# Optimization experiments

Measured on AMD Instinct MI355X. Metric: run time of the kernel, lower is better.

Reference implementation:

```python
import jax, jax.numpy as jnp
import numpy as np

T, B, IN_DIM = 8192, 4, 512
D_V, D_K, CHUNK = 512, 64, 128
EPS = 1e-8


def setup_inputs() -> dict:
    key = jax.random.key(0)
    ks = jax.random.split(key, 9)
    s = 0.02
    return {
        "x": jax.random.normal(ks[0], (T, B, IN_DIM), jnp.float32),
        "Wv": jax.random.normal(ks[1], (D_V, IN_DIM), jnp.float32) * s,
        "bv": jnp.zeros((D_V,), jnp.float32),
        "Wk": jax.random.normal(ks[2], (D_K, IN_DIM), jnp.float32) * s,
        "bk": jnp.zeros((D_K,), jnp.float32),
        "Wq": jax.random.normal(ks[3], (D_K, IN_DIM), jnp.float32) * s,
        "bq": jnp.zeros((D_K,), jnp.float32),
        "Wa": jax.random.normal(ks[4], (D_K, IN_DIM), jnp.float32) * s,
        "ba": jnp.zeros((D_K,), jnp.float32),
    }


def reference(x, Wv, bv, Wk, bk, Wq, bq, Wa, ba):
    # Projections: x (T, B, in_dim)
    v = x @ Wv.T + bv                      # (T, B, d)
    k = x @ Wk.T + bk                      # (T, B, n)
    q = x @ Wq.T + bq                      # (T, B, n)
    alpha = jax.nn.sigmoid(x @ Wa.T + ba)  # (T, B, n) decay gates

    Tt, Bb = x.shape[0], x.shape[1]
    C = CHUNK
    nC = Tt // C  # T assumed divisible by chunk size

    def to_chunks(a):
        return a.reshape(nC, C, Bb, a.shape[-1])

    vs, ks_, qs, als = to_chunks(v), to_chunks(k), to_chunks(q), to_chunks(alpha)
    causal = jnp.tril(jnp.ones((C, C), dtype=bool))  # (C, C)

    def body(S, inp):
        v_ch, k_ch, q_ch, a_ch = inp  # each (C, B, .)
        # Cumulative decay product within chunk (clamped as in the original)
        p = jnp.cumprod(jnp.maximum(a_ch, EPS), axis=0)      # (C, B, n)
        q_t = q_ch * p                                        # (C, B, n)
        k_t = k_ch / (p + EPS)                                # (C, B, n)
        # Intra-chunk causal attention scores
        A = jnp.einsum('tbn,sbn->bts', q_t, k_t)              # (B, C, C)
        A = jnp.where(causal[None, :, :], A, jnp.zeros((), A.dtype))
        y = jnp.einsum('bts,sbd->tbd', A, v_ch)               # intra-chunk
        y = y + jnp.einsum('bdn,tbn->tbd', S, q_t)            # cross-chunk carry
        # State update to end of chunk
        p_end = p[-1]                                         # (B, n)
        S_writes = jnp.einsum('tbd,tbn->bdn', v_ch, k_t * p_end[None, :, :])
        S_new = S * p_end[:, None, :] + S_writes              # (B, d, n)
        return S_new, y

    S0 = jnp.zeros((Bb, D_V, D_K), x.dtype)
    _, ys = jax.lax.scan(body, S0, (vs, ks_, qs, als))        # ys: (nC, C, B, d)
    return ys.reshape(Tt, Bb, D_V)
```

## Files before the change

### kernel.cpp

```cpp
#include <hip/hip_runtime.h>
#include <math.h>

#define T_DIM 8192
#define B_DIM 4
#define INDIM 512
#define DV 512
#define DK 64
#define CHUNK 128
#define NCH (T_DIM / CHUNK)
#define ROWS (T_DIM * B_DIM)
#define NPAD 768
#define KCAT 192
#define EPSF 1e-8f

typedef float float4_t __attribute__((ext_vector_type(4)));
typedef short short8_t __attribute__((ext_vector_type(8)));
typedef _Float16 half8_t __attribute__((ext_vector_type(8)));

__device__ inline unsigned short f2bf(float f) {
  unsigned int u = __float_as_uint(f);
  unsigned int r = (u + 0x7fffu + ((u >> 16) & 1u)) >> 16;
  return (unsigned short)r;
}
__device__ inline float bf2f(unsigned short h) {
  return __uint_as_float(((unsigned int)h) << 16);
}
__device__ inline unsigned short f2h(float f) {
  _Float16 h = (_Float16)f;
  unsigned short u;
  __builtin_memcpy(&u, &h, 2);
  return u;
}

__device__ inline void gload16(const void* g, void* l) {
  __builtin_amdgcn_global_load_lds(
      (const __attribute__((address_space(1))) void*)g,
      (__attribute__((address_space(3))) void*)l, 16, 0, 0);
}

__global__ __launch_bounds__(256) void cast_kernel(
    const float* __restrict__ x,
    const float* __restrict__ Wv, const float* __restrict__ Wk,
    const float* __restrict__ Wq, const float* __restrict__ Wa,
    const float* __restrict__ bv, const float* __restrict__ bk,
    const float* __restrict__ bq, const float* __restrict__ ba,
    unsigned short* __restrict__ xh, unsigned short* __restrict__ wh,
    float* __restrict__ bcat)
{
  if (blockIdx.x < 16384) {
    const size_t i4 = ((size_t)blockIdx.x * 256 + threadIdx.x) * 4;
    const float4 v = *(const float4*)&x[i4];
    ushort4 h;
    h.x = f2h(v.x); h.y = f2h(v.y); h.z = f2h(v.z); h.w = f2h(v.w);
    *(ushort4*)&xh[i4] = h;
  } else {
    const int t = (blockIdx.x - 16384) * 256 + threadIdx.x;
    const size_t i4 = (size_t)t * 4;
    const int row = (int)(i4 >> 9);
    const int col = (int)(i4 & 511);
    float4 v = {0.f, 0.f, 0.f, 0.f};
    if (row < 512)      v = *(const float4*)&Wv[(size_t)row * INDIM + col];
    else if (row < 576) v = *(const float4*)&Wk[(size_t)(row - 512) * INDIM + col];
    else if (row < 640) v = *(const float4*)&Wq[(size_t)(row - 576) * INDIM + col];
    else if (row < 704) v = *(const float4*)&Wa[(size_t)(row - 640) * INDIM + col];
    ushort4 h;
    h.x = f2h(v.x); h.y = f2h(v.y); h.z = f2h(v.z); h.w = f2h(v.w);
    *(ushort4*)&wh[i4] = h;
    if (t < NPAD) {
      float b = 0.f;
      if (t < 512)      b = bv[t];
      else if (t < 576) b = bk[t - 512];
      else if (t < 640) b = bq[t - 576];
      else if (t < 704) b = ba[t - 640];
      bcat[t] = b;
    }
  }
}

__global__ __launch_bounds__(256) void proj_mfma_kernel(
    const unsigned short* __restrict__ xh, const unsigned short* __restrict__ wh,
    const float* __restrict__ bcat,
    unsigned short* __restrict__ Bt_h, unsigned short* __restrict__ Bt_l,
    float* __restrict__ k_ws, float* __restrict__ q_ws,
    float* __restrict__ a_ws)
{
  __shared__ __align__(16) _Float16 Ah[3][128 * 32];
  __shared__ __align__(16) _Float16 Bh[3][128 * 32];

  const int d     = blockIdx.x;
  const int grp   = d >> 3;
  const int ytile = (d & 7) * 32 + grp / 6;
  const int xtile = grp % 6;
  const int r0 = ytile * 128;
  const int c0 = xtile * 128;

  const int tid  = threadIdx.x;
  const int wave = tid >> 6, lane = tid & 63;
  const int wm   = (wave & 1) * 64, wn = (wave >> 1) * 64;
  const int fm   = lane & 15;
  const int fk   = (lane >> 4) * 8;
  const int g    = lane >> 4;

  float4_t acc[4][4];
#pragma unroll
  for (int i = 0; i < 4; ++i)
#pragma unroll
    for (int j = 0; j < 4; ++j) acc[i][j] = (float4_t)0.0f;

  const int srow = tid >> 2;
  const int scol = (((tid & 3) ^ (srow & 3)) * 8);

  const unsigned short* pA0 = xh + (size_t)(r0 + srow) * INDIM + scol;
  const unsigned short* pA1 = xh + (size_t)(r0 + 64 + srow) * INDIM + scol;
  const unsigned short* pB0 = wh + (size_t)(c0 + srow) * INDIM + scol;
  const unsigned short* pB1 = wh + (size_t)(c0 + 64 + srow) * INDIM + scol;

  auto stage = [&](int buf, int k0) {
    gload16(pA0 + k0, &Ah[buf][tid * 8]);
    gload16(pA1 + k0, &Ah[buf][(256 + tid) * 8]);
    gload16(pB0 + k0, &Bh[buf][tid * 8]);
    gload16(pB1 + k0, &Bh[buf][(256 + tid) * 8]);
  };

  auto compute = [&](int buf) {
    half8_t a[4], b[4];
#pragma unroll
    for (int i = 0; i < 4; ++i) {
      const int r = wm + i * 16 + fm;
      a[i] = *(const half8_t*)&Ah[buf][r * 32 + ((g ^ (r & 3)) << 3)];
    }
#pragma unroll
    for (int j = 0; j < 4; ++j) {
      const int r = wn + j * 16 + fm;
      b[j] = *(const half8_t*)&Bh[buf][r * 32 + ((g ^ (r & 3)) << 3)];
    }
    __builtin_amdgcn_s_setprio(1);
#pragma unroll
    for (int i = 0; i < 4; ++i)
#pragma unroll
      for (int j = 0; j < 4; ++j)
        acc[i][j] = __builtin_amdgcn_mfma_f32_16x16x32_f16(a[i], b[j], acc[i][j], 0, 0, 0);
    __builtin_amdgcn_s_setprio(0);
  };

  stage(0, 0);
  stage(1, 32);
  int cur = 0;
  for (int t = 0; t < 14; ++t) {
    stage((cur + 2) % 3, (t + 2) * 32);
    asm volatile("s_waitcnt vmcnt(8)" ::: "memory");
    __builtin_amdgcn_s_barrier();
    compute(cur);
    __builtin_amdgcn_s_barrier();
    cur = (cur + 1) % 3;
  }
  asm volatile("s_waitcnt vmcnt(4)" ::: "memory");
  __builtin_amdgcn_s_barrier();
  compute(cur);
  cur = (cur + 1) % 3;
  asm volatile("s_waitcnt vmcnt(0)" ::: "memory");
  __builtin_amdgcn_s_barrier();
  compute(cur);

  if (xtile < 4) {
    unsigned int* Thl = (unsigned int*)&Ah[0][0];
    const int t0 = r0 >> 2;
    const int cb0 = (t0 >> 7) * 4;
    const int s0 = t0 & 127;
    __syncthreads();
    for (int bb = 0; bb < 4; ++bb) {
#pragma unroll
      for (int j = 0; j < 4; ++j) {
        const int d_loc = wn + j * 16 + fm;
        const float bias = bcat[c0 + d_loc];
#pragma unroll
        for (int i = 0; i < 4; ++i) {
          const int trow = (wm >> 2) + i * 4 + g;
          const float val = acc[i][j][bb] + bias;
          const unsigned short h = f2bf(val);
          const unsigned short l = f2bf(val - bf2f(h));
          Thl[d_loc * 34 + trow] = (unsigned int)h | ((unsigned int)l << 16);
        }
      }
      __syncthreads();
#pragma unroll
      for (int q2 = 0; q2 < 4; ++q2) {
        const int task = q2 * 256 + tid;
        const int dd = task >> 3;
        const int tq = task & 7;
        const unsigned int* p = &Thl[dd * 34 + tq * 4];
        const unsigned int w0 = p[0], w1 = p[1], w2 = p[2], w3 = p[3];
        ushort4 hh, ll;
        hh.x = (unsigned short)w0; ll.x = (unsigned short)(w0 >> 16);
        hh.y = (unsigned short)w1; ll.y = (unsigned short)(w1 >> 16);
        hh.z = (unsigned short)w2; ll.z = (unsigned short)(w2 >> 16);
        hh.w = (unsigned short)w3; ll.w = (unsigned short)(w3 >> 16);
        const size_t oa = ((size_t)(cb0 + bb) * DV + c0 + dd) * CHUNK + s0 + tq * 4;
        *(ushort4*)&Bt_h[oa] = hh;
        *(ushort4*)&Bt_l[oa] = ll;
      }
      __syncthreads();
    }
  } else {
#pragma unroll
    for (int j = 0; j < 4; ++j) {
      const int col = c0 + wn + j * 16 + fm;
      if (col >= 704) continue;
      const float bias = bcat[col];
#pragma unroll
      for (int i = 0; i < 4; ++i) {
#pragma unroll
        for (int r = 0; r < 4; ++r) {
          const int row = r0 + wm + i * 16 + g * 4 + r;
          const float val = acc[i][j][r] + bias;
          if (col < 576) {
            k_ws[(size_t)row * DK + col - 512] = val;
          } else if (col < 640) {
            q_ws[(size_t)row * DK + col - 576] = val;
          } else {
            a_ws[(size_t)row * DK + col - 640] = 1.0f / (1.0f + expf(-val));
          }
        }
      }
    }
  }
}

__global__ __launch_bounds__(512) void prep_kernel(
    const float* __restrict__ a_ws, const float* __restrict__ k_ws,
    const float* __restrict__ q_ws,
    unsigned short* __restrict__ Acat_h, unsigned short* __restrict__ Acat_l,
    unsigned short* __restrict__ kT_h, unsigned short* __restrict__ kT_l,
    float* __restrict__ pend)
{
  __shared__ float pal[CHUNK][DK];
  __shared__ __align__(16) unsigned short Aq_h[128 * 64];
  __shared__ __align__(16) unsigned short Aq_l[128 * 64];
  __shared__ __align__(16) unsigned short Bk_h[128 * 64];
  __shared__ __align__(16) unsigned short Bk_l[128 * 64];

  const int bd = blockIdx.x;
  const int l  = (bd & 7) * 32 + (bd >> 3);
  const int c = l >> 2, b = l & 3;
  const int cb = c * B_DIM + b;
  const int tid = threadIdx.x;
  const int wave = tid >> 6, lane = tid & 63;
  const int wm = (wave & 1) * 64, wn = (wave >> 1) * 32;
  const int fm = lane & 15;
  const int fk = (lane >> 4) * 8;
  const int g  = lane >> 4;

#pragma unroll
  for (int i = 0; i < 4; ++i) {
    const int f = (i * 512 + tid) * 4;
    const int t = f >> 6, n0 = f & 63;
    const float4 av = *(const float4*)&a_ws[(size_t)(c * CHUNK + t) * 256 + b * 64 + n0];
    *(float4*)&pal[t][n0] = av;
  }
  __syncthreads();

  if (tid < 64) {
    float p = 1.0f;
#pragma unroll 4
    for (int t = 0; t < CHUNK; ++t) {
      p *= fmaxf(pal[t][tid], EPSF);
      pal[t][tid] = p;
    }
    pend[c * 256 + b * 64 + tid] = p;
  }
  __syncthreads();

#pragma unroll
  for (int i = 0; i < 4; ++i) {
    const int f = (i * 512 + tid) * 4;
    const int t = f >> 6, n0 = f & 63;
    const float4 qv = *(const float4*)&q_ws[(size_t)(c * CHUNK + t) * 256 + b * 64 + n0];
    const size_t qa = ((size_t)cb * CHUNK + t) * KCAT + 128 + n0;
    float q0 = qv.x * pal[t][n0 + 0];
    float q1 = qv.y * pal[t][n0 + 1];
    float q2 = qv.z * pal[t][n0 + 2];
    float q3 = qv.w * pal[t][n0 + 3];
    ushort4 h, l4;
    h.x = f2bf(q0); l4.x = f2bf(q0 - bf2f(h.x));
    h.y = f2bf(q1); l4.y = f2bf(q1 - bf2f(h.y));
    h.z = f2bf(q2); l4.z = f2bf(q2 - bf2f(h.z));
    h.w = f2bf(q3); l4.w = f2bf(q3 - bf2f(h.w));
    *(ushort4*)&Acat_h[qa] = h;
    *(ushort4*)&Acat_l[qa] = l4;
    const int wi = t * 64 + (n0 ^ ((t & 7) << 3));
    *(ushort4*)&Aq_h[wi] = h;
    *(ushort4*)&Aq_l[wi] = l4;
  }

#pragma unroll
  for (int i = 0; i < 4; ++i) {
    const int f = (i * 512 + tid) * 4;
    const int t = f >> 6, n0 = f & 63;
    const float4 kv = *(const float4*)&k_ws[(size_t)(c * CHUNK + t) * 256 + b * 64 + n0];
    float k0 = kv.x / (pal[t][n0 + 0] + EPSF);
    float k1 = kv.y / (pal[t][n0 + 1] + EPSF);
    float k2 = kv.z / (pal[t][n0 + 2] + EPSF);
    float k3 = kv.w / (pal[t][n0 + 3] + EPSF);
    ushort4 h, l4;
    h.x = f2bf(k0); l4.x = f2bf(k0 - bf2f(h.x));
    h.y = f2bf(k1); l4.y = f2bf(k1 - bf2f(h.y));
    h.z = f2bf(k2); l4.z = f2bf(k2 - bf2f(h.z));
    h.w = f2bf(k3); l4.w = f2bf(k3 - bf2f(h.w));
    const int wi = t * 64 + (n0 ^ ((t & 7) << 3));
    *(ushort4*)&Bk_h[wi] = h;
    *(ushort4*)&Bk_l[wi] = l4;
  }
  __syncthreads();

#pragma unroll
  for (int it = 0; it < 2; ++it) {
    const int task = it * 512 + tid;
    const int n  = task >> 4;
    const int tg = task & 15;
    ushort4 h0, h1, l0, l1;
    unsigned short hh[8], ll[8];
#pragma unroll
    for (int e = 0; e < 8; ++e) {
      const int wi = (tg * 8 + e) * 64 + (n ^ (e << 3));
      hh[e] = Bk_h[wi];
      ll[e] = Bk_l[wi];
    }
    h0.x = hh[0]; h0.y = hh[1]; h0.z = hh[2]; h0.w = hh[3];
    h1.x = hh[4]; h1.y = hh[5]; h1.z = hh[6]; h1.w = hh[7];
    l0.x = ll[0]; l0.y = ll[1]; l0.z = ll[2]; l0.w = ll[3];
    l1.x = ll[4]; l1.y = ll[5]; l1.z = ll[6]; l1.w = ll[7];
    const size_t oa = ((size_t)cb * DK + n) * CHUNK + tg * 8;
    *(ushort4*)&kT_h[oa]     = h0;
    *(ushort4*)&kT_h[oa + 4] = h1;
    *(ushort4*)&kT_l[oa]     = l0;
    *(ushort4*)&kT_l[oa + 4] = l1;
  }

  float4_t acc[4][2];
#pragma unroll
  for (int i = 0; i < 4; ++i)
#pragma unroll
    for (int j = 0; j < 2; ++j) acc[i][j] = (float4_t)0.0f;

#pragma unroll
  for (int ksub = 0; ksub < 2; ++ksub) {
    short8_t a_hi[4], a_lo[4], b_hi[2], b_lo[2];
#pragma unroll
    for (int i = 0; i < 4; ++i) {
      const int r = wm + i * 16 + fm;
      const int ar = r * 64 + ((ksub * 32 + fk) ^ ((r & 7) << 3));
      a_hi[i] = *(const short8_t*)&Aq_h[ar];
      a_lo[i] = *(const short8_t*)&Aq_l[ar];
    }
#pragma unroll
    for (int j = 0; j < 2; ++j) {
      const int r = wn + j * 16 + fm;
      const int br = r * 64 + ((ksub * 32 + fk) ^ ((r & 7) << 3));
      b_hi[j] = *(const short8_t*)&Bk_h[br];
      b_lo[j] = *(const short8_t*)&Bk_l[br];
    }
    __builtin_amdgcn_s_setprio(1);
#pragma unroll
    for (int i = 0; i < 4; ++i)
#pragma unroll
      for (int j = 0; j < 2; ++j) {
        acc[i][j] = __builtin_amdgcn_mfma_f32_16x16x32_bf16(a_hi[i], b_hi[j], acc[i][j], 0, 0, 0);
        acc[i][j] = __builtin_amdgcn_mfma_f32_16x16x32_bf16(a_lo[i], b_hi[j], acc[i][j], 0, 0, 0);
        acc[i][j] = __builtin_amdgcn_mfma_f32_16x16x32_bf16(a_hi[i], b_lo[j], acc[i][j], 0, 0, 0);
      }
    __builtin_amdgcn_s_setprio(0);
  }

#pragma unroll
  for (int j = 0; j < 2; ++j) {
    const int s = wn + j * 16 + fm;
#pragma unroll
    for (int i = 0; i < 4; ++i) {
#pragma unroll
      for (int r = 0; r < 4; ++r) {
        const int t = wm + i * 16 + g * 4 + r;
        const float vv = (s <= t) ? acc[i][j][r] : 0.0f;
        const unsigned short h = f2bf(vv);
        const size_t oa = ((size_t)cb * CHUNK + t) * KCAT + s;
        Acat_h[oa] = h;
        Acat_l[oa] = f2bf(vv - bf2f(h));
      }
    }
  }
}

__global__ __launch_bounds__(256) void wchunk_mfma_kernel(
    const unsigned short* __restrict__ Bt_h, const unsigned short* __restrict__ Bt_l,
    const unsigned short* __restrict__ kT_h, const unsigned short* __restrict__ kT_l,
    const float* __restrict__ pend, float* __restrict__ W_ws)
{
  __shared__ __align__(16) unsigned short Ah[128 * 32];
  __shared__ __align__(16) unsigned short Al[128 * 32];
  __shared__ __align__(16) unsigned short Kh[64 * 128];
  __shared__ __align__(16) unsigned short Kl[64 * 128];

  const int bd = blockIdx.x;
  const int u  = (bd & 7) * 128 + (bd >> 3);
  const int cb = u >> 2;
  const int dt = u & 3;
  const int tid  = threadIdx.x;
  const int wave = tid >> 6, lane = tid & 63;
  const int wm   = (wave & 1) * 64;
  const int wn   = (wave >> 1) * 32;
  const int fm   = lane & 15;
  const int fk   = (lane >> 4) * 8;
  const int g    = lane >> 4;

  const unsigned short* Ab_h = Bt_h + ((size_t)cb * DV + dt * 128) * CHUNK;
  const unsigned short* Ab_l = Bt_l + ((size_t)cb * DV + dt * 128) * CHUNK;
  const unsigned short* Kb_h = kT_h + (size_t)cb * DK * CHUNK;
  const unsigned short* Kb_l = kT_l + (size_t)cb * DK * CHUNK;

#pragma unroll
  for (int it = 0; it < 4; ++it) {
    const int tk = it * 256 + tid;
    const int n = tk >> 4, slot = tk & 15;
    gload16(&Kb_h[(size_t)n * CHUNK + ((slot ^ (n & 15)) << 3)], &Kh[tk * 8]);
    gload16(&Kb_l[(size_t)n * CHUNK + ((slot ^ (n & 15)) << 3)], &Kl[tk * 8]);
  }

  float4_t acc[4][2];
#pragma unroll
  for (int i = 0; i < 4; ++i)
#pragma unroll
    for (int j = 0; j < 2; ++j) acc[i][j] = (float4_t)0.0f;

  for (int ks = 0; ks < 4; ++ks) {
    const int k0 = ks * 32;
#pragma unroll
    for (int q = 0; q < 2; ++q) {
      const int flat = (q * 256 + tid) * 8;
      const int row = flat >> 5;
      const int col = (((tid & 3) ^ ((tid >> 2) & 3)) << 3);
      gload16(&Ab_h[(size_t)row * CHUNK + k0 + col], &Ah[flat]);
      gload16(&Ab_l[(size_t)row * CHUNK + k0 + col], &Al[flat]);
    }
    __syncthreads();

    short8_t a_hi[4], a_lo[4], b_hi[2], b_lo[2];
#pragma unroll
    for (int i = 0; i < 4; ++i) {
      const int r = wm + i * 16 + fm;
      const int ar = r * 32 + ((g ^ (r & 3)) << 3);
      a_hi[i] = *(const short8_t*)&Ah[ar];
      a_lo[i] = *(const short8_t*)&Al[ar];
    }
#pragma unroll
    for (int j = 0; j < 2; ++j) {
      const int n = wn + j * 16 + fm;
      const int slot = (k0 + fk) >> 3;
      const int addr = n * CHUNK + ((slot ^ (n & 15)) << 3);
      b_hi[j] = *(const short8_t*)&Kh[addr];
      b_lo[j] = *(const short8_t*)&Kl[addr];
    }
#pragma unroll
    for (int i = 0; i < 4; ++i)
#pragma unroll
      for (int j = 0; j < 2; ++j) {
        acc[i][j] = __builtin_amdgcn_mfma_f32_16x16x32_bf16(a_hi[i], b_hi[j], acc[i][j], 0, 0, 0);
        acc[i][j] = __builtin_amdgcn_mfma_f32_16x16x32_bf16(a_lo[i], b_hi[j], acc[i][j], 0, 0, 0);
        acc[i][j] = __builtin_amdgcn_mfma_f32_16x16x32_bf16(a_hi[i], b_lo[j], acc[i][j], 0, 0, 0);
      }
    __syncthreads();
  }

#pragma unroll
  for (int j = 0; j < 2; ++j) {
    const int n = wn + j * 16 + fm;
    const float pj = pend[(cb >> 2) * 256 + (cb & 3) * 64 + n];
#pragma unroll
    for (int i = 0; i < 4; ++i) {
#pragma unroll
      for (int r = 0; r < 4; ++r) {
        const int dd = dt * 128 + wm + i * 16 + (lane >> 4) * 4 + r;
        W_ws[((size_t)cb * DV + dd) * DK + n] = acc[i][j][r] * pj;
      }
    }
  }
}

__global__ __launch_bounds__(256) void scan_kernel(
    const float* __restrict__ W_ws, const float* __restrict__ pend,
    unsigned short* __restrict__ Sh, unsigned short* __restrict__ Sl)
{
  const int flat = blockIdx.x * 256 + threadIdx.x;
  const int n = flat & 63;
  const int b = flat >> 15;
  float s = 0.0f;
  float w0 = W_ws[flat];
  float w1 = W_ws[131072 + flat];
  for (int c = 0; c < NCH; c += 2) {
    const float wa = w0, wb = w1;
    if (c + 2 < NCH) w0 = W_ws[(size_t)(c + 2) * 131072 + flat];
    if (c + 3 < NCH) w1 = W_ws[(size_t)(c + 3) * 131072 + flat];
    unsigned short h = f2bf(s);
    Sh[(size_t)c * 131072 + flat] = h;
    Sl[(size_t)c * 131072 + flat] = f2bf(s - bf2f(h));
    s = s * pend[c * 256 + b * 64 + n] + wa;
    h = f2bf(s);
    Sh[(size_t)(c + 1) * 131072 + flat] = h;
    Sl[(size_t)(c + 1) * 131072 + flat] = f2bf(s - bf2f(h));
    s = s * pend[(c + 1) * 256 + b * 64 + n] + wb;
  }
}

__global__ __launch_bounds__(256) void out_mfma_kernel(
    const unsigned short* __restrict__ Acat_h, const unsigned short* __restrict__ Acat_l,
    const unsigned short* __restrict__ Bt_h, const unsigned short* __restrict__ Bt_l,
    const unsigned short* __restrict__ Sh, const unsigned short* __restrict__ Sl,
    float* __restrict__ out)
{
  __shared__ __align__(16) unsigned short Ah[128 * 64];
  __shared__ __align__(16) unsigned short Al[128 * 64];
  __shared__ __align__(16) unsigned short Bh[128 * 64];
  __shared__ __align__(16) unsigned short Bl[128 * 64];

  const int bd = blockIdx.x;
  const int cb = (bd >> 5) * 8 + (bd & 7);
  const int nt = (bd >> 3) & 3;
  const int c = cb >> 2, b = cb & 3;
  const int tid  = threadIdx.x;
  const int wave = tid >> 6, lane = tid & 63;
  const int wm   = (wave & 1) * 64, wn = (wave >> 1) * 64;
  const int fm   = lane & 15;
  const int fk   = (lane >> 4) * 8;

  const unsigned short* Ab_h = Acat_h + (size_t)cb * CHUNK * KCAT;
  const unsigned short* Ab_l = Acat_l + (size_t)cb * CHUNK * KCAT;
  const unsigned short* Bb_h = Bt_h + ((size_t)cb * DV + nt * 128) * CHUNK;
  const unsigned short* Bb_l = Bt_l + ((size_t)cb * DV + nt * 128) * CHUNK;
  const unsigned short* Sb_h = Sh + ((size_t)cb * DV + nt * 128) * DK;
  const unsigned short* Sb_l = Sl + ((size_t)cb * DV + nt * 128) * DK;

  const int srow = tid >> 3;
  const int scolB = (tid & 7) * 16;
  const int sc = (scolB ^ ((srow & 7) << 4)) >> 1;
  const int sdst = srow * 64 + (scolB >> 1);

  float4_t acc[4][4];
#pragma unroll
  for (int i = 0; i < 4; ++i)
#pragma unroll
    for (int j = 0; j < 4; ++j) acc[i][j] = (float4_t)0.0f;

  for (int ks = 0; ks < 3; ++ks) {
    const int k0 = ks * 64;
#pragma unroll
    for (int q = 0; q < 4; ++q) {
      const int row = q * 32 + srow;
      const int dst = q * 2048 + sdst;
      gload16(&Ab_h[(size_t)row * KCAT + k0 + sc], &Ah[dst]);
      gload16(&Ab_l[(size_t)row * KCAT + k0 + sc], &Al[dst]);
      if (ks < 2) {
        gload16(&Bb_h[(size_t)row * CHUNK + k0 + sc], &Bh[dst]);
        gload16(&Bb_l[(size_t)row * CHUNK + k0 + sc], &Bl[dst]);
      } else {
        gload16(&Sb_h[(size_t)row * DK + sc], &Bh[dst]);
        gload16(&Sb_l[(size_t)row * DK + sc], &Bl[dst]);
      }
    }
    __syncthreads();

#pragma unroll
    for (int ksub = 0; ksub < 2; ++ksub) {
      short8_t a_hi[4], a_lo[4], b_hi[4], b_lo[4];
#pragma unroll
      for (int i = 0; i < 4; ++i) {
        const int r = wm + i * 16 + fm;
        const int ar = r * 64 + ((ksub * 32 + fk) ^ ((r & 7) << 3));
        a_hi[i] = *(const short8_t*)&Ah[ar];
        a_lo[i] = *(const short8_t*)&Al[ar];
      }
#pragma unroll
      for (int j = 0; j < 4; ++j) {
        const int r = wn + j * 16 + fm;
        const int br = r * 64 + ((ksub * 32 + fk) ^ ((r & 7) << 3));
        b_hi[j] = *(const short8_t*)&Bh[br];
        b_lo[j] = *(const short8_t*)&Bl[br];
      }
      __builtin_amdgcn_s_setprio(1);
#pragma unroll
      for (int i = 0; i < 4; ++i)
#pragma unroll
        for (int j = 0; j < 4; ++j) {
          acc[i][j] = __builtin_amdgcn_mfma_f32_16x16x32_bf16(a_hi[i], b_hi[j], acc[i][j], 0, 0, 0);
          acc[i][j] = __builtin_amdgcn_mfma_f32_16x16x32_bf16(a_lo[i], b_hi[j], acc[i][j], 0, 0, 0);
          acc[i][j] = __builtin_amdgcn_mfma_f32_16x16x32_bf16(a_hi[i], b_lo[j], acc[i][j], 0, 0, 0);
        }
      __builtin_amdgcn_s_setprio(0);
    }
    __syncthreads();
  }

#pragma unroll
  for (int j = 0; j < 4; ++j) {
    const int d = nt * 128 + wn + j * 16 + fm;
#pragma unroll
    for (int i = 0; i < 4; ++i) {
#pragma unroll
      for (int r = 0; r < 4; ++r) {
        const int t = c * CHUNK + wm + i * 16 + (lane >> 4) * 4 + r;
        out[((size_t)t * B_DIM + b) * DV + d] = acc[i][j][r];
      }
    }
  }
}

extern "C" void kernel_launch(void* const* d_in, const int* in_sizes, int n_in,
                              void* d_out, int out_size, void* d_ws, size_t ws_size,
                              hipStream_t stream)
{
  const float* x  = (const float*)d_in[0];
  const float* Wv = (const float*)d_in[1];
  const float* bv = (const float*)d_in[2];
  const float* Wk = (const float*)d_in[3];
  const float* bk = (const float*)d_in[4];
  const float* Wq = (const float*)d_in[5];
  const float* bq = (const float*)d_in[6];
  const float* Wa = (const float*)d_in[7];
  const float* ba = (const float*)d_in[8];
  float* out = (float*)d_out;

  float* ws   = (float*)d_ws;
  unsigned short* Bt_h = (unsigned short*)ws;
  unsigned short* Bt_l = Bt_h + (size_t)NCH * B_DIM * DV * CHUNK;
  float* k_ws = ws + (size_t)ROWS * DV;
  float* a_ws = k_ws + (size_t)ROWS * DK;
  float* pend = a_ws + (size_t)ROWS * DK;
  float* W_ws = pend + NCH * B_DIM * DK;
  float* bcat = W_ws + (size_t)NCH * B_DIM * DV * DK;
  unsigned short* Acat_h = (unsigned short*)(bcat + NPAD);
  unsigned short* Acat_l = Acat_h + (size_t)NCH * B_DIM * CHUNK * KCAT;
  unsigned short* uni = Acat_l + (size_t)NCH * B_DIM * CHUNK * KCAT;
  unsigned short* xh = uni;
  unsigned short* wh = xh + (size_t)ROWS * INDIM;
  float* q_ws = (float*)(uni + (size_t)18 * 1024 * 1024);
  unsigned short* kT_h = (unsigned short*)(q_ws + (size_t)ROWS * DK);
  unsigned short* kT_l = kT_h + (size_t)NCH * B_DIM * DK * CHUNK;
  unsigned short* S_h = uni;
  unsigned short* S_l = S_h + (size_t)NCH * B_DIM * DV * DK;

  cast_kernel<<<16384 + 384, 256, 0, stream>>>(
      x, Wv, Wk, Wq, Wa, bv, bk, bq, ba, xh, wh, bcat);
  proj_mfma_kernel<<<(ROWS / 128) * (NPAD / 128), 256, 0, stream>>>(
      xh, wh, bcat, Bt_h, Bt_l, k_ws, q_ws, a_ws);
  prep_kernel<<<NCH * B_DIM, 512, 0, stream>>>(
      a_ws, k_ws, q_ws, Acat_h, Acat_l, kT_h, kT_l, pend);
  wchunk_mfma_kernel<<<NCH * B_DIM * 4, 256, 0, stream>>>(
      Bt_h, Bt_l, kT_h, kT_l, pend, W_ws);
  scan_kernel<<<(B_DIM * DV * DK) / 256, 256, 0, stream>>>(
      W_ws, pend, S_h, S_l);
  out_mfma_kernel<<<NCH * B_DIM * 4, 256, 0, stream>>>(
      Acat_h, Acat_l, Bt_h, Bt_l, S_h, S_l, out);
}
```

Baseline: 268.2 us.

## Double-buffer LDS staging in wchunk and out MFMA kernels

Both the W-chunk and output MFMA kernels now use double-buffered LDS tiles with explicit vmcnt waits and raw barriers, so global-to-LDS loads for the next K-slice are in flight while the current slice is being multiplied. The output kernel also moves from 64-wide K slices to 32-wide slices with a 6-step, two-ahead prefetch schedule and a simpler XOR swizzle. The wchunk kernel gains setprio around its MFMA block. This hides global load latency at the cost of more barriers and reliance on hand-counted vmcnt values being correct.

```diff
diff --git a/kernel.cpp b/kernel.cpp
--- a/kernel.cpp
+++ b/kernel.cpp
@@ -98,7 +98,6 @@
   const int wave = tid >> 6, lane = tid & 63;
   const int wm   = (wave & 1) * 64, wn = (wave >> 1) * 64;
   const int fm   = lane & 15;
-  const int fk   = (lane >> 4) * 8;
   const int g    = lane >> 4;
 
   float4_t acc[4][4];
@@ -394,8 +393,8 @@
     const unsigned short* __restrict__ kT_h, const unsigned short* __restrict__ kT_l,
     const float* __restrict__ pend, float* __restrict__ W_ws)
 {
-  __shared__ __align__(16) unsigned short Ah[128 * 32];
-  __shared__ __align__(16) unsigned short Al[128 * 32];
+  __shared__ __align__(16) unsigned short Ah[2][128 * 32];
+  __shared__ __align__(16) unsigned short Al[2][128 * 32];
   __shared__ __align__(16) unsigned short Kh[64 * 128];
   __shared__ __align__(16) unsigned short Kl[64 * 128];
 
@@ -416,6 +415,17 @@
   const unsigned short* Kb_h = kT_h + (size_t)cb * DK * CHUNK;
   const unsigned short* Kb_l = kT_l + (size_t)cb * DK * CHUNK;
 
+  const int srow = tid >> 2;
+  const int scol = (((tid & 3) ^ (srow & 3)) * 8);
+
+  auto stageA = [&](int buf, int ks) {
+    const int k0 = ks * 32;
+    gload16(&Ab_h[(size_t)srow * CHUNK + k0 + scol], &Ah[buf][tid * 8]);
+    gload16(&Ab_h[(size_t)(srow + 64) * CHUNK + k0 + scol], &Ah[buf][(256 + tid) * 8]);
+    gload16(&Ab_l[(size_t)srow * CHUNK + k0 + scol], &Al[buf][tid * 8]);
+    gload16(&Ab_l[(size_t)(srow + 64) * CHUNK + k0 + scol], &Al[buf][(256 + tid) * 8]);
+  };
+
 #pragma unroll
   for (int it = 0; it < 4; ++it) {
     const int tk = it * 256 + tid;
@@ -423,6 +433,7 @@
     gload16(&Kb_h[(size_t)n * CHUNK + ((slot ^ (n & 15)) << 3)], &Kh[tk * 8]);
     gload16(&Kb_l[(size_t)n * CHUNK + ((slot ^ (n & 15)) << 3)], &Kl[tk * 8]);
   }
+  stageA(0, 0);
 
   float4_t acc[4][2];
 #pragma unroll
@@ -431,24 +442,23 @@
     for (int j = 0; j < 2; ++j) acc[i][j] = (float4_t)0.0f;
 
   for (int ks = 0; ks < 4; ++ks) {
+    if (ks + 1 < 4) {
+      stageA((ks + 1) & 1, ks + 1);
+      asm volatile("s_waitcnt vmcnt(4)" ::: "memory");
+    } else {
+      asm volatile("s_waitcnt vmcnt(0)" ::: "memory");
+    }
+    __builtin_amdgcn_s_barrier();
+
     const int k0 = ks * 32;
-#pragma unroll
-    for (int q = 0; q < 2; ++q) {
-      const int flat = (q * 256 + tid) * 8;
-      const int row = flat >> 5;
-      const int col = (((tid & 3) ^ ((tid >> 2) & 3)) << 3);
-      gload16(&Ab_h[(size_t)row * CHUNK + k0 + col], &Ah[flat]);
-      gload16(&Ab_l[(size_t)row * CHUNK + k0 + col], &Al[flat]);
-    }
-    __syncthreads();
-
+    const int buf = ks & 1;
     short8_t a_hi[4], a_lo[4], b_hi[2], b_lo[2];
 #pragma unroll
     for (int i = 0; i < 4; ++i) {
       const int r = wm + i * 16 + fm;
       const int ar = r * 32 + ((g ^ (r & 3)) << 3);
-      a_hi[i] = *(const short8_t*)&Ah[ar];
-      a_lo[i] = *(const short8_t*)&Al[ar];
+      a_hi[i] = *(const short8_t*)&Ah[buf][ar];
+      a_lo[i] = *(const short8_t*)&Al[buf][ar];
     }
 #pragma unroll
     for (int j = 0; j < 2; ++j) {
@@ -458,6 +468,7 @@
       b_hi[j] = *(const short8_t*)&Kh[addr];
       b_lo[j] = *(const short8_t*)&Kl[addr];
     }
+    __builtin_amdgcn_s_setprio(1);
 #pragma unroll
     for (int i = 0; i < 4; ++i)
 #pragma unroll
@@ -466,7 +477,8 @@
         acc[i][j] = __builtin_amdgcn_mfma_f32_16x16x32_bf16(a_lo[i], b_hi[j], acc[i][j], 0, 0, 0);
         acc[i][j] = __builtin_amdgcn_mfma_f32_16x16x32_bf16(a_hi[i], b_lo[j], acc[i][j], 0, 0, 0);
       }
-    __syncthreads();
+    __builtin_amdgcn_s_setprio(0);
+    __builtin_amdgcn_s_barrier();
   }
 
 #pragma unroll
@@ -515,10 +527,10 @@
     const unsigned short* __restrict__ Sh, const unsigned short* __restrict__ Sl,
     float* __restrict__ out)
 {
-  __shared__ __align__(16) unsigned short Ah[128 * 64];
-  __shared__ __align__(16) unsigned short Al[128 * 64];
-  __shared__ __align__(16) unsigned short Bh[128 * 64];
-  __shared__ __align__(16) unsigned short Bl[128 * 64];
+  __shared__ __align__(16) unsigned short Ah[2][128 * 32];
+  __shared__ __align__(16) unsigned short Al[2][128 * 32];
+  __shared__ __align__(16) unsigned short Bh[2][128 * 32];
+  __shared__ __align__(16) unsigned short Bl[2][128 * 32];
 
   const int bd = blockIdx.x;
   const int cb = (bd >> 5) * 8 + (bd & 7);
@@ -528,7 +540,7 @@
   const int wave = tid >> 6, lane = tid & 63;
   const int wm   = (wave & 1) * 64, wn = (wave >> 1) * 64;
   const int fm   = lane & 15;
-  const int fk   = (lane >> 4) * 8;
+  const int g    = lane >> 4;
 
   const unsigned short* Ab_h = Acat_h + (size_t)cb * CHUNK * KCAT;
   const unsigned short* Ab_l = Acat_l + (size_t)cb * CHUNK * KCAT;
@@ -537,10 +549,28 @@
   const unsigned short* Sb_h = Sh + ((size_t)cb * DV + nt * 128) * DK;
   const unsigned short* Sb_l = Sl + ((size_t)cb * DV + nt * 128) * DK;
 
-  const int srow = tid >> 3;
-  const int scolB = (tid & 7) * 16;
-  const int sc = (scolB ^ ((srow & 7) << 4)) >> 1;
-  const int sdst = srow * 64 + (scolB >> 1);
+  const int srow = tid >> 2;
+  const int scol = (((tid & 3) ^ (srow & 3)) * 8);
+
+  auto stage = [&](int buf, int t) {
+    const int k0 = t * 32;
+    gload16(&Ab_h[(size_t)srow * KCAT + k0 + scol], &Ah[buf][tid * 8]);
+    gload16(&Ab_h[(size_t)(srow + 64) * KCAT + k0 + scol], &Ah[buf][(256 + tid) * 8]);
+    gload16(&Ab_l[(size_t)srow * KCAT + k0 + scol], &Al[buf][tid * 8]);
+    gload16(&Ab_l[(size_t)(srow + 64) * KCAT + k0 + scol], &Al[buf][(256 + tid) * 8]);
+    if (t < 4) {
+      gload16(&Bb_h[(size_t)srow * CHUNK + k0 + scol], &Bh[buf][tid * 8]);
+      gload16(&Bb_h[(size_t)(srow + 64) * CHUNK + k0 + scol], &Bh[buf][(256 + tid) * 8]);
+      gload16(&Bb_l[(size_t)srow * CHUNK + k0 + scol], &Bl[buf][tid * 8]);
+      gload16(&Bb_l[(size_t)(srow + 64) * CHUNK + k0 + scol], &Bl[buf][(256 + tid) * 8]);
+    } else {
+      const int k0s = k0 - 128;
+      gload16(&Sb_h[(size_t)srow * DK + k0s + scol], &Bh[buf][tid * 8]);
+      gload16(&Sb_h[(size_t)(srow + 64) * DK + k0s + scol], &Bh[buf][(256 + tid) * 8]);
+      gload16(&Sb_l[(size_t)srow * DK + k0s + scol], &Bl[buf][tid * 8]);
+      gload16(&Sb_l[(size_t)(srow + 64) * DK + k0s + scol], &Bl[buf][(256 + tid) * 8]);
+    }
+  };
 
   float4_t acc[4][4];
 #pragma unroll
@@ -548,53 +578,45 @@
 #pragma unroll
     for (int j = 0; j < 4; ++j) acc[i][j] = (float4_t)0.0f;
 
-  for (int ks = 0; ks < 3; ++ks) {
-    const int k0 = ks * 64;
-#pragma unroll
-    for (int q = 0; q < 4; ++q) {
-      const int row = q * 32 + srow;
-      const int dst = q * 2048 + sdst;
-      gload16(&Ab_h[(size_t)row * KCAT + k0 + sc], &Ah[dst]);
-      gload16(&Ab_l[(size_t)row * KCAT + k0 + sc], &Al[dst]);
-      if (ks < 2) {
-        gload16(&Bb_h[(size_t)row * CHUNK + k0 + sc], &Bh[dst]);
-        gload16(&Bb_l[(size_t)row * CHUNK + k0 + sc], &Bl[dst]);
-      } else {
-        gload16(&Sb_h[(size_t)row * DK + sc], &Bh[dst]);
-        gload16(&Sb_l[(size_t)row * DK + sc], &Bl[dst]);
-      }
-    }
-    __syncthreads();
-
-#pragma unroll
-    for (int ksub = 0; ksub < 2; ++ksub) {
-      short8_t a_hi[4], a_lo[4], b_hi[4], b_lo[4];
-#pragma unroll
-      for (int i = 0; i < 4; ++i) {
-        const int r = wm + i * 16 + fm;
-        const int ar = r * 64 + ((ksub * 32 + fk) ^ ((r & 7) << 3));
-        a_hi[i] = *(const short8_t*)&Ah[ar];
-        a_lo[i] = *(const short8_t*)&Al[ar];
-      }
+  auto compute = [&](int buf) {
+    short8_t a_hi[4], a_lo[4], b_hi[4], b_lo[4];
+#pragma unroll
+    for (int i = 0; i < 4; ++i) {
+      const int r = wm + i * 16 + fm;
+      const int ar = r * 32 + ((g ^ (r & 3)) << 3);
+      a_hi[i] = *(const short8_t*)&Ah[buf][ar];
+      a_lo[i] = *(const short8_t*)&Al[buf][ar];
+    }
+#pragma unroll
+    for (int j = 0; j < 4; ++j) {
+      const int r = wn + j * 16 + fm;
+      const int br = r * 32 + ((g ^ (r & 3)) << 3);
+      b_hi[j] = *(const short8_t*)&Bh[buf][br];
+      b_lo[j] = *(const short8_t*)&Bl[buf][br];
+    }
+    __builtin_amdgcn_s_setprio(1);
+#pragma unroll
+    for (int i = 0; i < 4; ++i)
 #pragma unroll
       for (int j = 0; j < 4; ++j) {
-        const int r = wn + j * 16 + fm;
-        const int br = r * 64 + ((ksub * 32 + fk) ^ ((r & 7) << 3));
-        b_hi[j] = *(const short8_t*)&Bh[br];
-        b_lo[j] = *(const short8_t*)&Bl[br];
-      }
-      __builtin_amdgcn_s_setprio(1);
-#pragma unroll
-      for (int i = 0; i < 4; ++i)
-#pragma unroll
-        for (int j = 0; j < 4; ++j) {
-          acc[i][j] = __builtin_amdgcn_mfma_f32_16x16x32_bf16(a_hi[i], b_hi[j], acc[i][j], 0, 0, 0);
-          acc[i][j] = __builtin_amdgcn_mfma_f32_16x16x32_bf16(a_lo[i], b_hi[j], acc[i][j], 0, 0, 0);
-          acc[i][j] = __builtin_amdgcn_mfma_f32_16x16x32_bf16(a_hi[i], b_lo[j], acc[i][j], 0, 0, 0);
-        }
-      __builtin_amdgcn_s_setprio(0);
-    }
-    __syncthreads();
+        acc[i][j] = __builtin_amdgcn_mfma_f32_16x16x32_bf16(a_hi[i], b_hi[j], acc[i][j], 0, 0, 0);
+        acc[i][j] = __builtin_amdgcn_mfma_f32_16x16x32_bf16(a_lo[i], b_hi[j], acc[i][j], 0, 0, 0);
+        acc[i][j] = __builtin_amdgcn_mfma_f32_16x16x32_bf16(a_hi[i], b_lo[j], acc[i][j], 0, 0, 0);
+      }
+    __builtin_amdgcn_s_setprio(0);
+  };
+
+  stage(0, 0);
+  stage(1, 1);
+  int cur = 0;
+  for (int t = 0; t < 6; ++t) {
+    if (t < 5) asm volatile("s_waitcnt vmcnt(8)" ::: "memory");
+    else       asm volatile("s_waitcnt vmcnt(0)" ::: "memory");
+    __builtin_amdgcn_s_barrier();
+    compute(cur);
+    __builtin_amdgcn_s_barrier();
+    if (t + 2 < 6) stage(cur, t + 2);
+    cur ^= 1;
   }
 
 #pragma unroll
```

New measurement: 267.7 us. Within noise of the previous version (-0.2%).
